# Performance work log

Hardware: AMD Instinct MI355X
Metric: run time of the kernel (lower is better)

Reference implementation:

```python
import jax, jax.numpy as jnp
import numpy as np

HID = 1024   # hidden_size
HEADS = 16   # multi_head
DH = 64      # hidden_size_head
FF = 4096    # ff_size
EPS = 1e-6   # LayerNorm epsilon
NEG = -1e9


def setup_inputs() -> dict:
    key = jax.random.key(0)
    ks = jax.random.split(key, 24)
    B, LI, LQ, LK = 16, 512, 64, 128
    s = 0.02

    def w(k, shape):
        return jax.random.normal(k, shape, jnp.float32) * s

    return {
        "img_feat": jax.random.normal(ks[0], (B, LI, HID), jnp.float32),
        "ques": jax.random.normal(ks[1], (B, LQ, HID), jnp.float32),
        "kg": jax.random.normal(ks[2], (B, LK, HID), jnp.float32),
        "ques_mask": jax.random.randint(ks[3], (B, LQ), 0, 2, jnp.int32),
        "kg_mask": jax.random.randint(ks[4], (B, LK), 0, 2, jnp.int32),
        # stacked params for the 3 MHAtt blocks; torch Linear weight layout [out, in]
        "att_qw": w(ks[5], (3, HID, HID)), "att_qb": jnp.zeros((3, HID), jnp.float32),
        "att_kw": w(ks[6], (3, HID, HID)), "att_kb": jnp.zeros((3, HID), jnp.float32),
        "att_vw": w(ks[7], (3, HID, HID)), "att_vb": jnp.zeros((3, HID), jnp.float32),
        "att_ow": w(ks[8], (3, HID, HID)), "att_ob": jnp.zeros((3, HID), jnp.float32),
        "ffn_w1": w(ks[9], (FF, HID)), "ffn_b1": jnp.zeros((FF,), jnp.float32),
        "ffn_w2": w(ks[10], (HID, FF)), "ffn_b2": jnp.zeros((HID,), jnp.float32),
        "ln_g": jnp.ones((4, HID), jnp.float32), "ln_b": jnp.zeros((4, HID), jnp.float32),
    }


def _ln(x, g, b):
    m = jnp.mean(x, axis=-1, keepdims=True)
    v = jnp.mean(jnp.square(x - m), axis=-1, keepdims=True)
    return g * (x - m) / jnp.sqrt(v + EPS) + b


def _mha(v_in, k_in, q_in, mask, qw, qb, kw, kb, vw, vb, ow, ob):
    B = q_in.shape[0]

    def proj(x, wt, bi):  # [B,S,H] -> [B,heads,S,DH]
        y = jnp.einsum('bsh,oh->bso', x, wt) + bi
        return y.reshape(B, -1, HEADS, DH).transpose(0, 2, 1, 3)

    q = proj(q_in, qw, qb)
    k = proj(k_in, kw, kb)
    v = proj(v_in, vw, vb)
    scores = jnp.einsum('bhqd,bhkd->bhqk', q, k) / jnp.sqrt(jnp.float32(DH))
    if mask is not None:
        scores = jnp.where(mask[:, None, None, :] == 1, NEG, scores)
    a = jax.nn.softmax(scores, axis=-1)  # dropout is identity at eval
    o = jnp.einsum('bhqk,bhkd->bhqd', a, v).transpose(0, 2, 1, 3).reshape(B, -1, HID)
    return jnp.einsum('bsh,oh->bso', o, ow) + ob


def reference(img_feat, ques, kg, ques_mask, kg_mask,
              att_qw, att_qb, att_kw, att_kb, att_vw, att_vb, att_ow, att_ob,
              ffn_w1, ffn_b1, ffn_w2, ffn_b2, ln_g, ln_b):
    x = img_feat
    # self-attention on image features (no mask)
    x = _ln(x + _mha(x, x, x, None,
                     att_qw[0], att_qb[0], att_kw[0], att_kb[0],
                     att_vw[0], att_vb[0], att_ow[0], att_ob[0]), ln_g[0], ln_b[0])
    # cross-attention to question
    x = _ln(x + _mha(ques, ques, x, ques_mask,
                     att_qw[1], att_qb[1], att_kw[1], att_kb[1],
                     att_vw[1], att_vb[1], att_ow[1], att_ob[1]), ln_g[1], ln_b[1])
    # cross-attention to knowledge graph facts
    x = _ln(x + _mha(kg, kg, x, kg_mask,
                     att_qw[2], att_qb[2], att_kw[2], att_kb[2],
                     att_vw[2], att_vb[2], att_ow[2], att_ob[2]), ln_g[2], ln_b[2])
    # FFN: Linear -> ReLU -> Linear (dropout identity at eval)
    h = jax.nn.relu(jnp.einsum('bsh,fh->bsf', x, ffn_w1) + ffn_b1)
    f = jnp.einsum('bsf,hf->bsh', h, ffn_w2) + ffn_b2
    x = _ln(x + f, ln_g[3], ln_b[3])
    return x
```

## Files before the change

kernel.cpp:

```cpp
#include <hip/hip_runtime.h>
#include <math.h>

#define HIDN 1024
#define NHEADS 16
#define DHEAD 64
#define FFD 4096
#define LN_EPS 1e-6f
#define NEGV -1e9f

typedef __bf16 bf16_t;
typedef __bf16 bf16x8 __attribute__((ext_vector_type(8)));
typedef float f32x4 __attribute__((ext_vector_type(4)));
typedef unsigned short ushort8 __attribute__((ext_vector_type(8)));
typedef unsigned short ushort4v __attribute__((ext_vector_type(4)));

__device__ __forceinline__ unsigned short f2bf(float f) {
    unsigned u = __float_as_uint(f);
    return (unsigned short)((u + 0x7FFFu + ((u >> 16) & 1u)) >> 16);
}
__device__ __forceinline__ float bf2f(unsigned short u) {
    return __uint_as_float((unsigned)u << 16);
}
__device__ __forceinline__ void gld16(const void* g, void* l) {
    __builtin_amdgcn_global_load_lds(
        (const __attribute__((address_space(1))) void*)g,
        (__attribute__((address_space(3))) void*)l, 16, 0, 0);
}

template<int RELU>
__global__ __launch_bounds__(256)
void gemm_mfma(const bf16_t* __restrict__ A, const bf16_t* __restrict__ W,
               const float* __restrict__ ba, const float* __restrict__ bb,
               const float* __restrict__ bc, const float* __restrict__ bd,
               unsigned short* __restrict__ Cb, int M, int N, int K)
{
    __shared__ __align__(16) bf16_t As[128 * 64];
    __shared__ __align__(16) bf16_t Bs[128 * 64];

    const int tid  = threadIdx.x;
    const int wid  = tid >> 6;
    const int lane = tid & 63;
    const int m0 = blockIdx.x * 128;
    const int n0 = blockIdx.y * 128;
    const int wm = (wid & 1) * 64;
    const int wn = (wid >> 1) * 64;

    const int sr = (wid << 3) + (lane >> 3);
    const int sk = (((lane & 7) ^ (lane >> 3)) * 8);
    const bf16_t* pa = A + (size_t)(m0 + sr) * K + sk;
    const bf16_t* pb = W + (size_t)(n0 + sr) * K + sk;
    bf16_t* lA = &As[(wid << 3) * 64];
    bf16_t* lB = &Bs[(wid << 3) * 64];

    const int lr  = lane & 15;
    const int hi_ = lane >> 4;
    const int ch0 = ((hi_ + 0) ^ (lane & 7)) * 8;
    const int ch1 = ((hi_ + 4) ^ (lane & 7)) * 8;
    const bf16_t* fa = &As[(wm + lr) * 64];
    const bf16_t* fb = &Bs[(wn + lr) * 64];

    f32x4 acc[4][4];
    #pragma unroll
    for (int i = 0; i < 4; ++i)
        #pragma unroll
        for (int j = 0; j < 4; ++j) acc[i][j] = (f32x4){0.f, 0.f, 0.f, 0.f};

    for (int k0 = 0; k0 < K; k0 += 64) {
        __syncthreads();
        #pragma unroll
        for (int c = 0; c < 4; ++c) {
            gld16(pa + (size_t)c * 32 * K + k0, lA + c * 32 * 64);
            gld16(pb + (size_t)c * 32 * K + k0, lB + c * 32 * 64);
        }
        asm volatile("s_waitcnt vmcnt(0)" ::: "memory");
        __syncthreads();
        #pragma unroll
        for (int kk = 0; kk < 2; ++kk) {
            const int ch = kk ? ch1 : ch0;
            bf16x8 a[4], b[4];
            #pragma unroll
            for (int i = 0; i < 4; ++i) {
                a[i] = *(const bf16x8*)(fa + i * 16 * 64 + ch);
                b[i] = *(const bf16x8*)(fb + i * 16 * 64 + ch);
            }
            #pragma unroll
            for (int i = 0; i < 4; ++i)
                #pragma unroll
                for (int j = 0; j < 4; ++j)
                    acc[i][j] = __builtin_amdgcn_mfma_f32_16x16x32_bf16(
                        a[i], b[j], acc[i][j], 0, 0, 0);
        }
    }

    const int seg = n0 >> 10;
    const float* bias = (seg == 0) ? ba : (seg == 1) ? bb : (seg == 2) ? bc : bd;
    const int nl = (n0 & 1023);
    const int er = wm + (lane >> 4) * 4;
    const int ec = wn + (lane & 15);
    float bv[4];
    #pragma unroll
    for (int j = 0; j < 4; ++j) bv[j] = bias[nl + ec + j * 16];
    #pragma unroll
    for (int i = 0; i < 4; ++i)
        #pragma unroll
        for (int j = 0; j < 4; ++j)
            #pragma unroll
            for (int r = 0; r < 4; ++r) {
                float v = acc[i][j][r] + bv[j];
                if (RELU) v = fmaxf(v, 0.f);
                Cb[(size_t)(m0 + er + i * 16 + r) * N + (n0 + ec + j * 16)] = f2bf(v);
            }
}

template<int HAS_MASK>
__global__ __launch_bounds__(256)
void attn_mfma(const bf16_t* __restrict__ Q, const bf16_t* __restrict__ K,
               const bf16_t* __restrict__ V, int qstride, int kvstride,
               const int* __restrict__ mask,
               unsigned short* __restrict__ O, int Lk)
{
    __shared__ __align__(16) unsigned short Ks[64][72];
    __shared__ __align__(16) unsigned short Vt[64][72];
    __shared__ __align__(16) unsigned short Ps[64][72];
    __shared__ int smask[64];

    const int tid  = threadIdx.x;
    const int wid  = tid >> 6;
    const int lane = tid & 63;
    const int lo   = lane & 15;
    const int hi   = lane >> 4;
    const int q0   = blockIdx.x * 64;
    const int h    = blockIdx.y;
    const int b    = blockIdx.z;
    const int Lq   = 512;

    bf16x8 qf[2];
    {
        const bf16_t* qp = Q + (size_t)(b*Lq + q0 + wid*16 + lo) * qstride + h*DHEAD + hi*8;
        qf[0] = *(const bf16x8*)qp;
        qf[1] = *(const bf16x8*)(qp + 32);
    }

    float mrun[4], lrun[4];
    f32x4 Oc[4];
    #pragma unroll
    for (int r = 0; r < 4; ++r) { mrun[r] = -INFINITY; lrun[r] = 0.f; }
    #pragma unroll
    for (int n = 0; n < 4; ++n) Oc[n] = (f32x4){0.f, 0.f, 0.f, 0.f};

    const int sr = tid >> 2;
    const int sc = (tid & 3) * 16;

    for (int k0 = 0; k0 < Lk; k0 += 64) {
        {
            const bf16_t* kp = K + (size_t)(b*Lk + k0 + sr) * kvstride + h*DHEAD + sc;
            *(bf16x8*)&Ks[sr][sc]     = *(const bf16x8*)kp;
            *(bf16x8*)&Ks[sr][sc + 8] = *(const bf16x8*)(kp + 8);
            const unsigned short* vp = (const unsigned short*)
                (V + (size_t)(b*Lk + k0 + sr) * kvstride + h*DHEAD + sc);
            ushort8 v0 = *(const ushort8*)vp;
            ushort8 v1 = *(const ushort8*)(vp + 8);
            #pragma unroll
            for (int t = 0; t < 8; ++t) {
                Vt[sc + t][sr]     = v0[t];
                Vt[sc + 8 + t][sr] = v1[t];
            }
            if (HAS_MASK && tid < 64) smask[tid] = mask[b*Lk + k0 + tid];
        }
        __syncthreads();

        f32x4 s[4];
        #pragma unroll
        for (int j = 0; j < 4; ++j) s[j] = (f32x4){0.f, 0.f, 0.f, 0.f};
        #pragma unroll
        for (int kk = 0; kk < 2; ++kk) {
            #pragma unroll
            for (int j = 0; j < 4; ++j) {
                bf16x8 bfrag = *(const bf16x8*)&Ks[j*16 + lo][kk*32 + hi*8];
                s[j] = __builtin_amdgcn_mfma_f32_16x16x32_bf16(qf[kk], bfrag, s[j], 0, 0, 0);
            }
        }
        #pragma unroll
        for (int j = 0; j < 4; ++j) {
            bool msk = HAS_MASK ? (smask[j*16 + lo] != 0) : false;
            #pragma unroll
            for (int r = 0; r < 4; ++r) {
                float sv = s[j][r] * 0.125f;
                s[j][r] = msk ? NEGV : sv;
            }
        }

        #pragma unroll
        for (int r = 0; r < 4; ++r) {
            float tm = fmaxf(fmaxf(s[0][r], s[1][r]), fmaxf(s[2][r], s[3][r]));
            #pragma unroll
            for (int m = 1; m < 16; m <<= 1) tm = fmaxf(tm, __shfl_xor(tm, m));
            float mnew = fmaxf(mrun[r], tm);
            float f = __expf(mrun[r] - mnew);
            float ps = 0.f;
            #pragma unroll
            for (int j = 0; j < 4; ++j) {
                float p = __expf(s[j][r] - mnew);
                s[j][r] = p;
                ps += p;
            }
            #pragma unroll
            for (int m = 1; m < 16; m <<= 1) ps += __shfl_xor(ps, m);
            lrun[r] = lrun[r] * f + ps;
            mrun[r] = mnew;
            #pragma unroll
            for (int n = 0; n < 4; ++n) Oc[n][r] *= f;
            #pragma unroll
            for (int j = 0; j < 4; ++j)
                Ps[wid*16 + hi*4 + r][j*16 + lo] = f2bf(s[j][r]);
        }

        #pragma unroll
        for (int kk = 0; kk < 2; ++kk) {
            bf16x8 pa = *(const bf16x8*)&Ps[wid*16 + lo][kk*32 + hi*8];
            #pragma unroll
            for (int n = 0; n < 4; ++n) {
                bf16x8 vf = *(const bf16x8*)&Vt[n*16 + lo][kk*32 + hi*8];
                Oc[n] = __builtin_amdgcn_mfma_f32_16x16x32_bf16(pa, vf, Oc[n], 0, 0, 0);
            }
        }
        __syncthreads();
    }

    #pragma unroll
    for (int r = 0; r < 4; ++r) {
        float inv = 1.f / lrun[r];
        const size_t row = (size_t)(b*Lq + q0 + wid*16 + hi*4 + r) * HIDN + h*DHEAD;
        #pragma unroll
        for (int n = 0; n < 4; ++n)
            O[row + n*16 + lo] = f2bf(Oc[n][r] * inv);
    }
}

template<int WF32, int WBF>
__global__ __launch_bounds__(256)
void ln_res_b(const unsigned short* __restrict__ X, const unsigned short* __restrict__ R,
              const float* __restrict__ G, const float* __restrict__ Bv,
              unsigned short* __restrict__ OutB, float* __restrict__ OutF)
{
    const int row = blockIdx.x;
    const int tid = threadIdx.x;
    const size_t base = (size_t)row * HIDN + tid * 4;
    ushort4v xv = *(const ushort4v*)(X + base);
    ushort4v rv = *(const ushort4v*)(R + base);
    float y[4];
    #pragma unroll
    for (int t = 0; t < 4; ++t) y[t] = bf2f(xv[t]) + bf2f(rv[t]);
    float s1 = y[0] + y[1] + y[2] + y[3];
    float s2 = y[0]*y[0] + y[1]*y[1] + y[2]*y[2] + y[3]*y[3];
    #pragma unroll
    for (int m = 1; m < 64; m <<= 1) {
        s1 += __shfl_xor(s1, m);
        s2 += __shfl_xor(s2, m);
    }
    __shared__ float red1[4], red2[4];
    const int wave = tid >> 6, lane = tid & 63;
    if (lane == 0) { red1[wave] = s1; red2[wave] = s2; }
    __syncthreads();
    s1 = red1[0] + red1[1] + red1[2] + red1[3];
    s2 = red2[0] + red2[1] + red2[2] + red2[3];
    const float mean = s1 * (1.f / HIDN);
    const float var  = s2 * (1.f / HIDN) - mean * mean;
    const float inv  = rsqrtf(var + LN_EPS);
    float4 gv = *(const float4*)(G + tid*4);
    float4 bv = *(const float4*)(Bv + tid*4);
    float o[4];
    o[0] = gv.x * (y[0]-mean) * inv + bv.x;
    o[1] = gv.y * (y[1]-mean) * inv + bv.y;
    o[2] = gv.z * (y[2]-mean) * inv + bv.z;
    o[3] = gv.w * (y[3]-mean) * inv + bv.w;
    if (WBF) {
        ushort4v ob;
        #pragma unroll
        for (int t = 0; t < 4; ++t) ob[t] = f2bf(o[t]);
        *(ushort4v*)(OutB + base) = ob;
    }
    if (WF32) {
        float4 of = {o[0], o[1], o[2], o[3]};
        *(float4*)(OutF + base) = of;
    }
}

__global__ __launch_bounds__(256)
void cvt_bf16(const float* __restrict__ in, unsigned short* __restrict__ out, int n8)
{
    int i = blockIdx.x * blockDim.x + threadIdx.x;
    const int stride = gridDim.x * blockDim.x;
    for (; i < n8; i += stride) {
        const float4* p = (const float4*)in + (size_t)i * 2;
        float4 a = p[0], b = p[1];
        ushort8 o;
        o[0] = f2bf(a.x); o[1] = f2bf(a.y); o[2] = f2bf(a.z); o[3] = f2bf(a.w);
        o[4] = f2bf(b.x); o[5] = f2bf(b.y); o[6] = f2bf(b.z); o[7] = f2bf(b.w);
        ((ushort8*)out)[i] = o;
    }
}

extern "C" void kernel_launch(void* const* d_in, const int* in_sizes, int n_in,
                              void* d_out, int out_size, void* d_ws, size_t ws_size,
                              hipStream_t stream)
{
    const float* img   = (const float*)d_in[0];
    const float* ques  = (const float*)d_in[1];
    const float* kg    = (const float*)d_in[2];
    const int*   qmask = (const int*)d_in[3];
    const int*   kmask = (const int*)d_in[4];
    const float* qw = (const float*)d_in[5];
    const float* qb = (const float*)d_in[6];
    const float* kw = (const float*)d_in[7];
    const float* kb = (const float*)d_in[8];
    const float* vw = (const float*)d_in[9];
    const float* vb = (const float*)d_in[10];
    const float* ow = (const float*)d_in[11];
    const float* ob = (const float*)d_in[12];
    const float* w1 = (const float*)d_in[13];
    const float* b1 = (const float*)d_in[14];
    const float* w2 = (const float*)d_in[15];
    const float* b2 = (const float*)d_in[16];
    const float* lng = (const float*)d_in[17];
    const float* lnb = (const float*)d_in[18];
    float* out = (float*)d_out;

    const int B = 16;
    const int NX = B * 512;
    const size_t WSTEP = (size_t)1024 * 1024;
    const size_t MB = (size_t)1 << 20;
    const size_t MELEM = (size_t)1024 * 1024;

    char* wsb = (char*)d_ws;
    unsigned short* xb    = (unsigned short*)(wsb);
    unsigned short* bM    = (unsigned short*)(wsb + 16*MB);
    unsigned short* bOb   = (unsigned short*)(wsb + 32*MB);
    unsigned short* quesb = (unsigned short*)(wsb + 48*MB);
    unsigned short* kgb   = (unsigned short*)(wsb + 50*MB);
    unsigned short* wcat  = (unsigned short*)(wsb + 56*MB);
    unsigned short* bQKV  = (unsigned short*)(wsb + 72*MB);
    unsigned short* bKV   = (unsigned short*)(wsb + 120*MB);
    unsigned short* hb    = (unsigned short*)(wsb + 128*MB);

    dim3 blk(256);
    auto cvt = [&](const float* src, unsigned short* dst, size_t n) {
        int n8 = (int)(n / 8);
        int grid = (n8 + 255) / 256; if (grid > 2048) grid = 2048;
        cvt_bf16<<<grid, blk, 0, stream>>>(src, dst, n8);
    };
    auto gemm = [&](const unsigned short* A, const unsigned short* W,
                    const float* ba, const float* bb_, const float* bc, const float* bd,
                    unsigned short* C, int M, int N, int K, int relu) {
        dim3 grid(M / 128, N / 128);
        if (relu) gemm_mfma<1><<<grid, blk, 0, stream>>>(
            (const bf16_t*)A, (const bf16_t*)W, ba, bb_, bc, bd, C, M, N, K);
        else      gemm_mfma<0><<<grid, blk, 0, stream>>>(
            (const bf16_t*)A, (const bf16_t*)W, ba, bb_, bc, bd, C, M, N, K);
    };

    cvt(img,  xb,    (size_t)NX * HIDN);
    cvt(ques, quesb, (size_t)B * 64 * HIDN);
    cvt(kg,   kgb,   (size_t)B * 128 * HIDN);

    const unsigned short* Akv[3] = {xb, quesb, kgb};
    const int Mkv[3] = {NX, B * 64, B * 128};
    const int Lk[3]  = {512, 64, 128};

    for (int t = 0; t < 3; ++t) {
        if (t == 0) {
            cvt(qw + t*WSTEP, wcat,           MELEM);
            cvt(kw + t*WSTEP, wcat + MELEM,   MELEM);
            cvt(vw + t*WSTEP, wcat + 2*MELEM, MELEM);
            gemm(xb, wcat, qb + t*1024, kb + t*1024, vb + t*1024, vb + t*1024,
                 bQKV, NX, 3072, 1024, 0);
            attn_mfma<0><<<dim3(8, NHEADS, B), blk, 0, stream>>>(
                (const bf16_t*)bQKV, (const bf16_t*)bQKV + 1024, (const bf16_t*)bQKV + 2048,
                3072, 3072, nullptr, bOb, Lk[t]);
        } else {
            cvt(qw + t*WSTEP, wcat, MELEM);
            gemm(xb, wcat, qb + t*1024, qb + t*1024, qb + t*1024, qb + t*1024,
                 bQKV, NX, 1024, 1024, 0);
            cvt(kw + t*WSTEP, wcat,         MELEM);
            cvt(vw + t*WSTEP, wcat + MELEM, MELEM);
            gemm(Akv[t], wcat, kb + t*1024, vb + t*1024, vb + t*1024, vb + t*1024,
                 bKV, Mkv[t], 2048, 1024, 0);
            attn_mfma<1><<<dim3(8, NHEADS, B), blk, 0, stream>>>(
                (const bf16_t*)bQKV, (const bf16_t*)bKV, (const bf16_t*)bKV + 1024,
                1024, 2048, (t == 1 ? qmask : kmask), bOb, Lk[t]);
        }
        cvt(ow + t*WSTEP, wcat, MELEM);
        gemm(bOb, wcat, ob + t*1024, ob + t*1024, ob + t*1024, ob + t*1024,
             bM, NX, 1024, 1024, 0);
        ln_res_b<0,1><<<NX, blk, 0, stream>>>(xb, bM, lng + t*1024, lnb + t*1024, xb, nullptr);
    }

    cvt(w1, wcat, (size_t)FFD * HIDN);
    gemm(xb, wcat, b1, b1 + 1024, b1 + 2048, b1 + 3072, hb, NX, FFD, 1024, 1);
    cvt(w2, wcat, (size_t)HIDN * FFD);
    gemm(hb, wcat, b2, b2, b2, b2, bM, NX, 1024, 4096, 0);
    ln_res_b<1,0><<<NX, blk, 0, stream>>>(xb, bM, lng + 3*1024, lnb + 3*1024, nullptr, out);
}
```

Measured before the change: 606.7 us.

## Double-buffer GEMM LDS tiles and batch all bf16 conversions into one launch

The GEMM now uses two LDS buffers and issues global-to-LDS loads for the next K tile before computing on the current one, overlapping memory latency with MFMA work. All fp32-to-bf16 conversions of weights and activations are merged into a single up-front launch with a per-unit pointer table, replacing many small conversion kernels spread through the pipeline. This doubles LDS use per GEMM block, which can lower occupancy, and it needs a larger workspace to hold every converted weight at once.

```diff
diff --git a/kernel.cpp b/kernel.cpp
--- a/kernel.cpp
+++ b/kernel.cpp
@@ -34,8 +34,8 @@
                const float* __restrict__ bc, const float* __restrict__ bd,
                unsigned short* __restrict__ Cb, int M, int N, int K)
 {
-    __shared__ __align__(16) bf16_t As[128 * 64];
-    __shared__ __align__(16) bf16_t Bs[128 * 64];
+    __shared__ __align__(16) bf16_t As[2][128 * 64];
+    __shared__ __align__(16) bf16_t Bs[2][128 * 64];
 
     const int tid  = threadIdx.x;
     const int wid  = tid >> 6;
@@ -49,15 +49,12 @@
     const int sk = (((lane & 7) ^ (lane >> 3)) * 8);
     const bf16_t* pa = A + (size_t)(m0 + sr) * K + sk;
     const bf16_t* pb = W + (size_t)(n0 + sr) * K + sk;
-    bf16_t* lA = &As[(wid << 3) * 64];
-    bf16_t* lB = &Bs[(wid << 3) * 64];
+    const int lofs = (wid << 3) * 64;
 
     const int lr  = lane & 15;
     const int hi_ = lane >> 4;
     const int ch0 = ((hi_ + 0) ^ (lane & 7)) * 8;
     const int ch1 = ((hi_ + 4) ^ (lane & 7)) * 8;
-    const bf16_t* fa = &As[(wm + lr) * 64];
-    const bf16_t* fb = &Bs[(wn + lr) * 64];
 
     f32x4 acc[4][4];
     #pragma unroll
@@ -65,15 +62,16 @@
         #pragma unroll
         for (int j = 0; j < 4; ++j) acc[i][j] = (f32x4){0.f, 0.f, 0.f, 0.f};
 
-    for (int k0 = 0; k0 < K; k0 += 64) {
-        __syncthreads();
+    auto stage = [&](int buf, int koff) {
         #pragma unroll
         for (int c = 0; c < 4; ++c) {
-            gld16(pa + (size_t)c * 32 * K + k0, lA + c * 32 * 64);
-            gld16(pb + (size_t)c * 32 * K + k0, lB + c * 32 * 64);
-        }
-        asm volatile("s_waitcnt vmcnt(0)" ::: "memory");
-        __syncthreads();
+            gld16(pa + (size_t)c * 32 * K + koff, &As[buf][lofs + c * 32 * 64]);
+            gld16(pb + (size_t)c * 32 * K + koff, &Bs[buf][lofs + c * 32 * 64]);
+        }
+    };
+    auto compute = [&](int buf) {
+        const bf16_t* fa = &As[buf][(wm + lr) * 64];
+        const bf16_t* fb = &Bs[buf][(wn + lr) * 64];
         #pragma unroll
         for (int kk = 0; kk < 2; ++kk) {
             const int ch = kk ? ch1 : ch0;
@@ -90,6 +88,21 @@
                     acc[i][j] = __builtin_amdgcn_mfma_f32_16x16x32_bf16(
                         a[i], b[j], acc[i][j], 0, 0, 0);
         }
+    };
+
+    stage(0, 0);
+    asm volatile("s_waitcnt vmcnt(0)" ::: "memory");
+    __syncthreads();
+
+    for (int k0 = 0; k0 < K; k0 += 128) {
+        if (k0 + 64 < K) stage(1, k0 + 64);
+        compute(0);
+        asm volatile("s_waitcnt vmcnt(0)" ::: "memory");
+        __syncthreads();
+        if (k0 + 128 < K) stage(0, k0 + 128);
+        compute(1);
+        asm volatile("s_waitcnt vmcnt(0)" ::: "memory");
+        __syncthreads();
     }
 
     const int seg = n0 >> 10;
@@ -286,19 +299,23 @@
     }
 }
 
+struct CvtArgs {
+    const float* src[32];
+    unsigned short* dst[32];
+};
+
 __global__ __launch_bounds__(256)
-void cvt_bf16(const float* __restrict__ in, unsigned short* __restrict__ out, int n8)
+void cvt_units(CvtArgs args)
 {
-    int i = blockIdx.x * blockDim.x + threadIdx.x;
-    const int stride = gridDim.x * blockDim.x;
-    for (; i < n8; i += stride) {
-        const float4* p = (const float4*)in + (size_t)i * 2;
-        float4 a = p[0], b = p[1];
-        ushort8 o;
-        o[0] = f2bf(a.x); o[1] = f2bf(a.y); o[2] = f2bf(a.z); o[3] = f2bf(a.w);
-        o[4] = f2bf(b.x); o[5] = f2bf(b.y); o[6] = f2bf(b.z); o[7] = f2bf(b.w);
-        ((ushort8*)out)[i] = o;
-    }
+    const float* s = args.src[blockIdx.y];
+    unsigned short* d = args.dst[blockIdx.y];
+    const int i = blockIdx.x * 256 + threadIdx.x;
+    const float4* p = (const float4*)s + (size_t)i * 2;
+    float4 a = p[0], b = p[1];
+    ushort8 o;
+    o[0] = f2bf(a.x); o[1] = f2bf(a.y); o[2] = f2bf(a.z); o[3] = f2bf(a.w);
+    o[4] = f2bf(b.x); o[5] = f2bf(b.y); o[6] = f2bf(b.z); o[7] = f2bf(b.w);
+    ((ushort8*)d)[i] = o;
 }
 
 extern "C" void kernel_launch(void* const* d_in, const int* in_sizes, int n_in,
@@ -338,17 +355,41 @@
     unsigned short* bOb   = (unsigned short*)(wsb + 32*MB);
     unsigned short* quesb = (unsigned short*)(wsb + 48*MB);
     unsigned short* kgb   = (unsigned short*)(wsb + 50*MB);
-    unsigned short* wcat  = (unsigned short*)(wsb + 56*MB);
-    unsigned short* bQKV  = (unsigned short*)(wsb + 72*MB);
-    unsigned short* bKV   = (unsigned short*)(wsb + 120*MB);
-    unsigned short* hb    = (unsigned short*)(wsb + 128*MB);
+    unsigned short* wa    = (unsigned short*)(wsb + 56*MB);
+    unsigned short* bQKV  = (unsigned short*)(wsb + 96*MB);
+    unsigned short* bKV   = (unsigned short*)(wsb + 144*MB);
+    unsigned short* hb    = (unsigned short*)(wsb + 96*MB);
+
+    CvtArgs ca;
+    int u = 0;
+    auto addu = [&](const float* src, int melems, unsigned short* dst) {
+        for (int i = 0; i < melems; ++i) {
+            ca.src[u] = src + (size_t)i * MELEM;
+            ca.dst[u] = dst + (size_t)i * MELEM;
+            ++u;
+        }
+    };
+    addu(qw + 0*WSTEP, 1, wa + 0*MELEM);
+    addu(kw + 0*WSTEP, 1, wa + 1*MELEM);
+    addu(vw + 0*WSTEP, 1, wa + 2*MELEM);
+    addu(qw + 1*WSTEP, 1, wa + 3*MELEM);
+    addu(kw + 1*WSTEP, 1, wa + 4*MELEM);
+    addu(vw + 1*WSTEP, 1, wa + 5*MELEM);
+    addu(qw + 2*WSTEP, 1, wa + 6*MELEM);
+    addu(kw + 2*WSTEP, 1, wa + 7*MELEM);
+    addu(vw + 2*WSTEP, 1, wa + 8*MELEM);
+    addu(ow + 0*WSTEP, 1, wa + 9*MELEM);
+    addu(ow + 1*WSTEP, 1, wa + 10*MELEM);
+    addu(ow + 2*WSTEP, 1, wa + 11*MELEM);
+    addu(w1, 4, wa + 12*MELEM);
+    addu(w2, 4, wa + 16*MELEM);
+    addu(img,  8, xb);
+    addu(ques, 1, quesb);
+    addu(kg,   2, kgb);
 
     dim3 blk(256);
-    auto cvt = [&](const float* src, unsigned short* dst, size_t n) {
-        int n8 = (int)(n / 8);
-        int grid = (n8 + 255) / 256; if (grid > 2048) grid = 2048;
-        cvt_bf16<<<grid, blk, 0, stream>>>(src, dst, n8);
-    };
+    cvt_units<<<dim3(512, u), blk, 0, stream>>>(ca);
+
     auto gemm = [&](const unsigned short* A, const unsigned short* W,
                     const float* ba, const float* bb_, const float* bc, const float* bd,
                     unsigned short* C, int M, int N, int K, int relu) {
@@ -359,45 +400,35 @@
             (const bf16_t*)A, (const bf16_t*)W, ba, bb_, bc, bd, C, M, N, K);
     };
 
-    cvt(img,  xb,    (size_t)NX * HIDN);
-    cvt(ques, quesb, (size_t)B * 64 * HIDN);
-    cvt(kg,   kgb,   (size_t)B * 128 * HIDN);
-
     const unsigned short* Akv[3] = {xb, quesb, kgb};
     const int Mkv[3] = {NX, B * 64, B * 128};
     const int Lk[3]  = {512, 64, 128};
 
     for (int t = 0; t < 3; ++t) {
         if (t == 0) {
-            cvt(qw + t*WSTEP, wcat,           MELEM);
-            cvt(kw + t*WSTEP, wcat + MELEM,   MELEM);
-            cvt(vw + t*WSTEP, wcat + 2*MELEM, MELEM);
-            gemm(xb, wcat, qb + t*1024, kb + t*1024, vb + t*1024, vb + t*1024,
+            gemm(xb, wa + 0*MELEM, qb + 0, kb + 0, vb + 0, vb + 0,
                  bQKV, NX, 3072, 1024, 0);
             attn_mfma<0><<<dim3(8, NHEADS, B), blk, 0, stream>>>(
                 (const bf16_t*)bQKV, (const bf16_t*)bQKV + 1024, (const bf16_t*)bQKV + 2048,
                 3072, 3072, nullptr, bOb, Lk[t]);
         } else {
-            cvt(qw + t*WSTEP, wcat, MELEM);
-            gemm(xb, wcat, qb + t*1024, qb + t*1024, qb + t*1024, qb + t*1024,
+            gemm(xb, wa + (t == 1 ? 3 : 6)*MELEM,
+                 qb + t*1024, qb + t*1024, qb + t*1024, qb + t*1024,
                  bQKV, NX, 1024, 1024, 0);
-            cvt(kw + t*WSTEP, wcat,         MELEM);
-            cvt(vw + t*WSTEP, wcat + MELEM, MELEM);
-            gemm(Akv[t], wcat, kb + t*1024, vb + t*1024, vb + t*1024, vb + t*1024,
+            gemm(Akv[t], wa + (t == 1 ? 4 : 7)*MELEM,
+                 kb + t*1024, vb + t*1024, vb + t*1024, vb + t*1024,
                  bKV, Mkv[t], 2048, 1024, 0);
             attn_mfma<1><<<dim3(8, NHEADS, B), blk, 0, stream>>>(
                 (const bf16_t*)bQKV, (const bf16_t*)bKV, (const bf16_t*)bKV + 1024,
                 1024, 2048, (t == 1 ? qmask : kmask), bOb, Lk[t]);
         }
-        cvt(ow + t*WSTEP, wcat, MELEM);
-        gemm(bOb, wcat, ob + t*1024, ob + t*1024, ob + t*1024, ob + t*1024,
+        gemm(bOb, wa + (9 + t)*MELEM,
+             ob + t*1024, ob + t*1024, ob + t*1024, ob + t*1024,
              bM, NX, 1024, 1024, 0);
         ln_res_b<0,1><<<NX, blk, 0, stream>>>(xb, bM, lng + t*1024, lnb + t*1024, xb, nullptr);
     }
 
-    cvt(w1, wcat, (size_t)FFD * HIDN);
-    gemm(xb, wcat, b1, b1 + 1024, b1 + 2048, b1 + 3072, hb, NX, FFD, 1024, 1);
-    cvt(w2, wcat, (size_t)HIDN * FFD);
-    gemm(hb, wcat, b2, b2, b2, b2, bM, NX, 1024, 4096, 0);
+    gemm(xb, wa + 12*MELEM, b1, b1 + 1024, b1 + 2048, b1 + 3072, hb, NX, FFD, 1024, 1);
+    gemm(hb, wa + 16*MELEM, b2, b2, b2, b2, bM, NX, 1024, 4096, 0);
     ln_res_b<1,0><<<NX, blk, 0, stream>>>(xb, bM, lng + 3*1024, lnb + 3*1024, nullptr, out);
 }
```

Result: faster. 517.9 us (-14.6%).
